# Kernel optimization log

Measured on AMD Instinct MI355X. Metric: run time of the kernel, lower is better.

Reference implementation:

```python
import jax, jax.numpy as jnp
import numpy as np
from jax import lax

B = 32768
N_INP = 256
N_HIDDEN = 1024
N_F = 256
N_ITERS = 100  # fixed-point solver iteration count in Convex


def _make_operators(n_f):
    # D = tridiag(-1, 2, -1) with first/last rows zeroed; mid = 0.5 * (sub+super diag ones)
    D = (-np.diag(np.ones(n_f - 1), -1) + 2 * np.diag(np.ones(n_f))
         - np.diag(np.ones(n_f - 1), 1)).astype(np.float32)
    D[0, :] = 0.0
    D[n_f - 1, :] = 0.0
    mid = 0.5 * (np.diag(np.ones(n_f - 1), -1) + np.diag(np.ones(n_f - 1), 1)).astype(np.float32)
    return jnp.asarray(D), jnp.asarray(mid)


def _convex(param):
    # param: [B, n_f]  (the torch code carries [B, n_f, 1]; column vec is equivalent)
    D, mid = _make_operators(param.shape[-1])

    def body(z, _):
        zx = z + param                       # [B, n_f]
        Dz = jnp.einsum('ij,bj->bi', D, zx)  # D @ zx
        mz = jnp.einsum('ij,bj->bi', mid, zx)
        dx = jnp.where(Dz > 0, zx - mz, 0.0)
        return zx - dx - param, None

    z0 = jnp.zeros_like(param)
    z_star, _ = lax.scan(body, z0, None, length=N_ITERS)
    return param + z_star  # Convex.forward: x + model(x)


def setup_inputs() -> dict:
    key = jax.random.key(0)
    k = jax.random.split(key, 5)
    x = jax.random.uniform(k[0], (B, N_INP + 1), dtype=jnp.float32)
    W1 = jax.random.normal(k[1], (N_HIDDEN, N_INP), dtype=jnp.float32) * 0.02
    b1 = jax.random.normal(k[2], (N_HIDDEN,), dtype=jnp.float32) * 0.02
    W2 = jax.random.normal(k[3], (N_F, N_HIDDEN), dtype=jnp.float32) * 0.02
    b2 = jax.random.normal(k[4], (N_F,), dtype=jnp.float32) * 0.02
    return {"x": x, "W1": W1, "b1": b1, "W2": W2, "b2": b2}


def reference(x, W1, b1, W2, b2):
    h = jax.nn.relu(x[..., :N_INP] @ W1.T + b1)     # [B, n_hidden]
    x_ = h @ W2.T + b2                              # [B, n_f]
    param = _convex(x_)                             # [B, n_f]
    # EvalConvex: round(query * (n_f - 1)) -> gather along feature dim
    idx = jnp.round(x[..., N_INP] * (N_F - 1)).astype(jnp.int32)  # [B]
    out = jnp.take_along_axis(param, idx[:, None], axis=1)        # [B, 1]
    return out.reshape(-1, 1, 1)                                  # [B, 1, 1]
```

## Files before the change

kernel.cpp:

```cpp
#include <hip/hip_runtime.h>
#include <stdint.h>

#define B_ROWS 32768
#define N_INP 256
#define N_HID 1024
#define NF 256
#define N_IT 100

typedef __attribute__((ext_vector_type(8))) _Float16 f16x8;
typedef __attribute__((ext_vector_type(4))) float f32x4;
typedef __attribute__((ext_vector_type(2))) _Float16 f16x2;
typedef float f32x4a __attribute__((ext_vector_type(4), aligned(4)));
typedef uint32_t u32;

__device__ __forceinline__ ushort f2h(float f) {
  _Float16 h = (_Float16)f;
  return *reinterpret_cast<ushort*>(&h);
}

__device__ __forceinline__ u32 pkh(float a, float b) {
  _Float16 ha = (_Float16)a, hb = (_Float16)b;
  return (u32)*reinterpret_cast<ushort*>(&ha) |
         ((u32)*reinterpret_cast<ushort*>(&hb) << 16);
}

__device__ __forceinline__ void async_copy16(const void* g, void* l) {
  __builtin_amdgcn_global_load_lds(
      (const __attribute__((address_space(1))) void*)g,
      (__attribute__((address_space(3))) void*)l, 16, 0, 0);
}

__device__ __forceinline__ f16x2 as_h2(u32 x) { return __builtin_bit_cast(f16x2, x); }
__device__ __forceinline__ u32 as_u32(f16x2 x) { return __builtin_bit_cast(u32, x); }
__device__ __forceinline__ f16x2 min2(f16x2 a, f16x2 b) {
  f16x2 r;
  asm("v_pk_min_f16 %0, %1, %2" : "=v"(r) : "v"(a), "v"(b));
  return r;
}

__global__ void prep_kernel(const float* __restrict__ x,
                            const float* __restrict__ W1,
                            const float* __restrict__ W2,
                            ushort* __restrict__ w1h,
                            ushort* __restrict__ w2h,
                            int* __restrict__ idx) {
  if (blockIdx.x < 256) {
    int t = blockIdx.x * 256 + threadIdx.x;
    float4 a = reinterpret_cast<const float4*>(W1)[t];
    float4 b = reinterpret_cast<const float4*>(W2)[t];
    reinterpret_cast<ushort4*>(w1h)[t] = make_ushort4(f2h(a.x), f2h(a.y), f2h(a.z), f2h(a.w));
    reinterpret_cast<ushort4*>(w2h)[t] = make_ushort4(f2h(b.x), f2h(b.y), f2h(b.z), f2h(b.w));
  } else {
    int r = (blockIdx.x - 256) * 256 + threadIdx.x;
    idx[r] = (int)rintf(x[(size_t)r * 257 + 256] * 255.0f);
  }
}

__global__ __launch_bounds__(256) void gemm1_x(
    const float* __restrict__ X,
    const ushort* __restrict__ Bw,
    const float* __restrict__ bias,
    ushort* __restrict__ C,
    int ntN) {
  __shared__ ushort As[2][128 * 64];
  __shared__ ushort Bs[2][128 * 64];
  const int t = threadIdx.x;
  const int w = t >> 6, l = t & 63;
  int bid = blockIdx.x;
  if (((int)gridDim.x & 7) == 0) {
    int cpx = (int)gridDim.x >> 3;
    bid = (bid & 7) * cpx + (bid >> 3);
  }
  const int tm = bid / ntN, tn = bid % ntN;
  const int wm = w >> 1, wn = w & 1;

  const float* Xb = X + (size_t)(tm * 128) * 257;
  const char* Bb = (const char*)(Bw + (size_t)tn * 128 * 256);
  const int sB = 512;
  const int lrow = l >> 3;
  const int lcol = (l & 7) * 16;

  const int ar0 = t >> 3;
  const int ak0 = (t & 7) * 8;

  f32x4a a0, a1, a2, a3, a4, a5, a6, a7;
#define LOADA(kt)                                                        \
  {                                                                      \
    const float* p0 = Xb + (size_t)ar0 * 257 + (kt) * 64 + ak0;          \
    const float* p1 = p0 + (size_t)32 * 257;                             \
    const float* p2 = p0 + (size_t)64 * 257;                             \
    const float* p3 = p0 + (size_t)96 * 257;                             \
    a0 = *(const f32x4a*)p0; a1 = *(const f32x4a*)(p0 + 4);              \
    a2 = *(const f32x4a*)p1; a3 = *(const f32x4a*)(p1 + 4);              \
    a4 = *(const f32x4a*)p2; a5 = *(const f32x4a*)(p2 + 4);              \
    a6 = *(const f32x4a*)p3; a7 = *(const f32x4a*)(p3 + 4);              \
  }
#define WRITEA(buf)                                                      \
  {                                                                      \
    uint4* d = (uint4*)((char*)&As[buf][0] + t * 16);                    \
    d[0]   = make_uint4(pkh(a0.x, a0.y), pkh(a0.z, a0.w),                \
                        pkh(a1.x, a1.y), pkh(a1.z, a1.w));               \
    d[256] = make_uint4(pkh(a2.x, a2.y), pkh(a2.z, a2.w),                \
                        pkh(a3.x, a3.y), pkh(a3.z, a3.w));               \
    d[512] = make_uint4(pkh(a4.x, a4.y), pkh(a4.z, a4.w),                \
                        pkh(a5.x, a5.y), pkh(a5.z, a5.w));               \
    d[768] = make_uint4(pkh(a6.x, a6.y), pkh(a6.z, a6.w),                \
                        pkh(a7.x, a7.y), pkh(a7.z, a7.w));               \
  }
#define STAGEB(kt, buf)                                                  \
  {                                                                      \
    const char* gb = Bb + lrow * sB + (kt) * 128 + lcol;                 \
    _Pragma("unroll") for (int i = 0; i < 4; ++i) {                      \
      int c = w * 4 + i;                                                 \
      async_copy16(gb + c * 8 * sB, (char*)&Bs[buf][0] + c * 1024);      \
    }                                                                    \
  }

  f32x4 acc[4][4];
#pragma unroll
  for (int i = 0; i < 4; ++i)
#pragma unroll
    for (int j = 0; j < 4; ++j) acc[i][j] = {0.f, 0.f, 0.f, 0.f};

  LOADA(0);
  STAGEB(0, 0);
  WRITEA(0);
  __syncthreads();

  const int arow = wm * 64 + (l & 15);
  const int brow = wn * 64 + (l & 15);
  const int koff = (l >> 4) * 8;

  for (int kt = 0; kt < 4; ++kt) {
    const int buf = kt & 1;
    if (kt < 3) {
      LOADA(kt + 1);
      STAGEB(kt + 1, buf ^ 1);
    }
#pragma unroll
    for (int ks = 0; ks < 2; ++ks) {
      f16x8 af[4], bfr[4];
#pragma unroll
      for (int mi = 0; mi < 4; ++mi)
        af[mi] = *(const f16x8*)&As[buf][(arow + mi * 16) * 64 + ks * 32 + koff];
#pragma unroll
      for (int ni = 0; ni < 4; ++ni)
        bfr[ni] = *(const f16x8*)&Bs[buf][(brow + ni * 16) * 64 + ks * 32 + koff];
#pragma unroll
      for (int mi = 0; mi < 4; ++mi)
#pragma unroll
        for (int ni = 0; ni < 4; ++ni)
          acc[mi][ni] = __builtin_amdgcn_mfma_f32_16x16x32_f16(
              af[mi], bfr[ni], acc[mi][ni], 0, 0, 0);
    }
    if (kt < 3) WRITEA(buf ^ 1);
    __syncthreads();
  }
#undef LOADA
#undef WRITEA
#undef STAGEB

  const int grow0 = tm * 128 + wm * 64 + (l >> 4) * 4;
  const int gcol0 = tn * 128 + wn * 64 + (l & 15);
#pragma unroll
  for (int ni = 0; ni < 4; ++ni) {
    const int col = gcol0 + ni * 16;
    const float bv = bias[col];
#pragma unroll
    for (int mi = 0; mi < 4; ++mi) {
      const int row = grow0 + mi * 16;
#pragma unroll
      for (int r = 0; r < 4; ++r) {
        float v = fmaxf(acc[mi][ni][r] + bv, 0.f);
        C[(size_t)(row + r) * N_HID + col] = f2h(v);
      }
    }
  }
}

__global__ __launch_bounds__(1024, 8) void gemm2_convex(
    const ushort* __restrict__ A,
    const ushort* __restrict__ Bw,
    const float* __restrict__ bias,
    const int* __restrict__ idxp,
    float* __restrict__ out) {
  __shared__ ushort smem[20480];
  const int tid = threadIdx.x;
  const int w = tid >> 6, l = tid & 63;
  const int wm = w >> 2, wn = w & 3;
  const int m0r = blockIdx.x * 64;

  f32x4 acc[4];
#pragma unroll
  for (int i = 0; i < 4; ++i) acc[i] = {0.f, 0.f, 0.f, 0.f};

  const int srow = tid >> 2;
  const int scs = (tid & 3) ^ ((srow >> 1) & 3);
  const ushort* gA = A + (size_t)(m0r + srow) * N_HID + scs * 8;
  const ushort* gB = Bw + (size_t)srow * N_HID + scs * 8;

#define STAGE(kt, buf)                                                  \
  {                                                                     \
    if (tid < 256) async_copy16(gA + (kt) * 32, smem + (buf) * 2048 + tid * 8); \
    async_copy16(gB + (kt) * 32, smem + 4096 + (buf) * 8192 + tid * 8); \
  }

  STAGE(0, 0);
  __syncthreads();

  const int arow = wm * 16 + (l & 15);
  const int brow0 = wn * 64 + (l & 15);
  const int kx = (((l >> 4) ^ ((l >> 1) & 3)) * 8);

  for (int kt = 0; kt < 32; ++kt) {
    const int buf = kt & 1;
    if (kt < 31) STAGE(kt + 1, buf ^ 1);
    f16x8 af = *(const f16x8*)(smem + buf * 2048 + arow * 32 + kx);
#pragma unroll
    for (int ni = 0; ni < 4; ++ni) {
      f16x8 bf = *(const f16x8*)(smem + 4096 + buf * 8192 + (brow0 + ni * 16) * 32 + kx);
      acc[ni] = __builtin_amdgcn_mfma_f32_16x16x32_f16(af, bf, acc[ni], 0, 0, 0);
    }
    __syncthreads();
  }
#undef STAGE

  {
    const int r0 = wm * 16 + (l >> 4) * 4;
    const int c0 = wn * 64 + (l & 15);
#pragma unroll
    for (int ni = 0; ni < 4; ++ni) {
      const int col = c0 + ni * 16;
      const float bv = bias[col];
#pragma unroll
      for (int r = 0; r < 4; ++r)
        smem[(r0 + r) * 256 + col] = f2h(acc[ni][r] + bv);
    }
  }
  __syncthreads();

  const int q = l & 15;
  const int row = w * 4 + (l >> 4);
  u32 w0, w1, w2, w3, w4, w5, w6, w7;
  {
    const uint4* src = reinterpret_cast<const uint4*>(smem + row * 256 + q * 16);
    uint4 v0 = src[0], v1 = src[1];
    w0 = v0.x; w1 = v0.y; w2 = v0.z; w3 = v0.w;
    w4 = v1.x; w5 = v1.y; w6 = v1.z; w7 = v1.w;
  }
  const int ii = idxp[m0r + row];
  const int upIdx = ((l - 1) & 63) * 4;
  const int dnIdx = ((l + 1) & 63) * 4;
  const bool fixP = (q == 0);
  const bool fixN = (q == 15);
  const f16x2 halfc = {(_Float16)0.5f, (_Float16)0.5f};

  u32 P = __builtin_amdgcn_ds_bpermute(upIdx, w7);
  u32 N = __builtin_amdgcn_ds_bpermute(dnIdx, w0);

#define AB(hi, lo) as_h2(__builtin_amdgcn_alignbit((hi), (lo), 16))
#define UPD(wj, sa, sb) wj = as_u32(min2(as_h2(wj), ((sa) + (sb)) * halfc))
#pragma unroll 2
  for (int it = 0; it < N_IT; ++it) {
    const u32 Pf = fixP ? 0x7C000000u : P;
    const u32 Nf = fixN ? 0x00007C00u : N;
    f16x2 s0 = AB(w0, Pf), s1 = AB(w1, w0), s2 = AB(w2, w1), s3 = AB(w3, w2);
    f16x2 s4 = AB(w4, w3), s5 = AB(w5, w4), s6 = AB(w6, w5), s7 = AB(w7, w6);
    f16x2 s8 = AB(Nf, w7);
    UPD(w7, s7, s8);
    UPD(w0, s0, s1);
    P = __builtin_amdgcn_ds_bpermute(upIdx, w7);
    N = __builtin_amdgcn_ds_bpermute(dnIdx, w0);
    UPD(w1, s1, s2); UPD(w2, s2, s3); UPD(w3, s3, s4);
    UPD(w4, s4, s5); UPD(w5, s5, s6); UPD(w6, s6, s7);
  }
#undef AB
#undef UPD

  const int sel = (ii >> 1) & 7;
  u32 a0 = (sel & 4) ? w4 : w0, a1 = (sel & 4) ? w5 : w1;
  u32 a2 = (sel & 4) ? w6 : w2, a3 = (sel & 4) ? w7 : w3;
  u32 b0 = (sel & 2) ? a2 : a0, b1 = (sel & 2) ? a3 : a1;
  u32 c0 = (sel & 1) ? b1 : b0;
  ushort hv = (ii & 1) ? (ushort)(c0 >> 16) : (ushort)(c0 & 0xffffu);
  float v = (float)__builtin_bit_cast(_Float16, hv);
  v = __shfl(v, (l & ~15) | (ii >> 4));
  if (q == 0) out[m0r + row] = v;
}

extern "C" void kernel_launch(void* const* d_in, const int* in_sizes, int n_in,
                              void* d_out, int out_size, void* d_ws, size_t ws_size,
                              hipStream_t stream) {
  const float* x = (const float*)d_in[0];
  const float* W1 = (const float*)d_in[1];
  const float* b1 = (const float*)d_in[2];
  const float* W2 = (const float*)d_in[3];
  const float* b2 = (const float*)d_in[4];
  float* out = (float*)d_out;

  char* ws = (char*)d_ws;
  ushort* w1h = (ushort*)ws;
  ushort* w2h = (ushort*)(ws + 524288);
  int*    idx = (int*)  (ws + 1048576);
  ushort* h   = (ushort*)(ws + 1179648);

  const size_t fixed = 1179648;
  int chunk = 2048;
  if (ws_size >= fixed + (size_t)32768 * 2048) chunk = 32768;
  else if (ws_size >= fixed + (size_t)16384 * 2048) chunk = 16384;
  else if (ws_size >= fixed + (size_t)8192 * 2048) chunk = 8192;
  else if (ws_size >= fixed + (size_t)4096 * 2048) chunk = 4096;

  prep_kernel<<<384, 256, 0, stream>>>(x, W1, W2, w1h, w2h, idx);

  for (int m0 = 0; m0 < B_ROWS; m0 += chunk) {
    int curM = (B_ROWS - m0 < chunk) ? (B_ROWS - m0) : chunk;
    dim3 g1((curM / 128) * (N_HID / 128));
    gemm1_x<<<g1, 256, 0, stream>>>(x + (size_t)m0 * 257, w1h, b1, h,
                                    N_HID / 128);
    gemm2_convex<<<curM / 64, 1024, 0, stream>>>(h, w2h, b2, idx + m0, out + m0);
  }
}
```

Before: 122.5 us.

## Merge GEMM1 and GEMM2+convex into one software-pipelined kernel over chunks

Replaces the separate gemm1 and gemm2_convex launches with a single kernel. Each launch runs gemm1 for chunk k and gemm2+convex for chunk k-1 at the same time, using a double-buffered hidden workspace. The goal is to overlap the ALU-heavy convex iteration with the MFMA/memory-bound first GEMM and to shrink chunk sizes for better L2 locality. Gemm1 is rewritten for 1024-thread blocks with smaller per-wave tiles (32x32) and swizzled LDS. The cost is extra launches (nch+1) and less register reuse per wave in gemm1.

After: 219.1 us. +78.8%, slower.

```diff
diff --git a/kernel.cpp b/kernel.cpp
--- a/kernel.cpp
+++ b/kernel.cpp
@@ -56,148 +56,34 @@
   }
 }
 
-__global__ __launch_bounds__(256) void gemm1_x(
-    const float* __restrict__ X,
-    const ushort* __restrict__ Bw,
-    const float* __restrict__ bias,
-    ushort* __restrict__ C,
-    int ntN) {
-  __shared__ ushort As[2][128 * 64];
-  __shared__ ushort Bs[2][128 * 64];
-  const int t = threadIdx.x;
-  const int w = t >> 6, l = t & 63;
-  int bid = blockIdx.x;
-  if (((int)gridDim.x & 7) == 0) {
-    int cpx = (int)gridDim.x >> 3;
-    bid = (bid & 7) * cpx + (bid >> 3);
-  }
-  const int tm = bid / ntN, tn = bid % ntN;
-  const int wm = w >> 1, wn = w & 1;
-
-  const float* Xb = X + (size_t)(tm * 128) * 257;
-  const char* Bb = (const char*)(Bw + (size_t)tn * 128 * 256);
-  const int sB = 512;
-  const int lrow = l >> 3;
-  const int lcol = (l & 7) * 16;
-
-  const int ar0 = t >> 3;
-  const int ak0 = (t & 7) * 8;
-
-  f32x4a a0, a1, a2, a3, a4, a5, a6, a7;
-#define LOADA(kt)                                                        \
-  {                                                                      \
-    const float* p0 = Xb + (size_t)ar0 * 257 + (kt) * 64 + ak0;          \
-    const float* p1 = p0 + (size_t)32 * 257;                             \
-    const float* p2 = p0 + (size_t)64 * 257;                             \
-    const float* p3 = p0 + (size_t)96 * 257;                             \
-    a0 = *(const f32x4a*)p0; a1 = *(const f32x4a*)(p0 + 4);              \
-    a2 = *(const f32x4a*)p1; a3 = *(const f32x4a*)(p1 + 4);              \
-    a4 = *(const f32x4a*)p2; a5 = *(const f32x4a*)(p2 + 4);              \
-    a6 = *(const f32x4a*)p3; a7 = *(const f32x4a*)(p3 + 4);              \
-  }
-#define WRITEA(buf)                                                      \
-  {                                                                      \
-    uint4* d = (uint4*)((char*)&As[buf][0] + t * 16);                    \
-    d[0]   = make_uint4(pkh(a0.x, a0.y), pkh(a0.z, a0.w),                \
-                        pkh(a1.x, a1.y), pkh(a1.z, a1.w));               \
-    d[256] = make_uint4(pkh(a2.x, a2.y), pkh(a2.z, a2.w),                \
-                        pkh(a3.x, a3.y), pkh(a3.z, a3.w));               \
-    d[512] = make_uint4(pkh(a4.x, a4.y), pkh(a4.z, a4.w),                \
-                        pkh(a5.x, a5.y), pkh(a5.z, a5.w));               \
-    d[768] = make_uint4(pkh(a6.x, a6.y), pkh(a6.z, a6.w),                \
-                        pkh(a7.x, a7.y), pkh(a7.z, a7.w));               \
-  }
-#define STAGEB(kt, buf)                                                  \
-  {                                                                      \
-    const char* gb = Bb + lrow * sB + (kt) * 128 + lcol;                 \
-    _Pragma("unroll") for (int i = 0; i < 4; ++i) {                      \
-      int c = w * 4 + i;                                                 \
-      async_copy16(gb + c * 8 * sB, (char*)&Bs[buf][0] + c * 1024);      \
-    }                                                                    \
-  }
-
-  f32x4 acc[4][4];
-#pragma unroll
-  for (int i = 0; i < 4; ++i)
-#pragma unroll
-    for (int j = 0; j < 4; ++j) acc[i][j] = {0.f, 0.f, 0.f, 0.f};
-
-  LOADA(0);
-  STAGEB(0, 0);
-  WRITEA(0);
-  __syncthreads();
-
-  const int arow = wm * 64 + (l & 15);
-  const int brow = wn * 64 + (l & 15);
-  const int koff = (l >> 4) * 8;
-
-  for (int kt = 0; kt < 4; ++kt) {
-    const int buf = kt & 1;
-    if (kt < 3) {
-      LOADA(kt + 1);
-      STAGEB(kt + 1, buf ^ 1);
-    }
-#pragma unroll
-    for (int ks = 0; ks < 2; ++ks) {
-      f16x8 af[4], bfr[4];
-#pragma unroll
-      for (int mi = 0; mi < 4; ++mi)
-        af[mi] = *(const f16x8*)&As[buf][(arow + mi * 16) * 64 + ks * 32 + koff];
-#pragma unroll
-      for (int ni = 0; ni < 4; ++ni)
-        bfr[ni] = *(const f16x8*)&Bs[buf][(brow + ni * 16) * 64 + ks * 32 + koff];
-#pragma unroll
-      for (int mi = 0; mi < 4; ++mi)
-#pragma unroll
-        for (int ni = 0; ni < 4; ++ni)
-          acc[mi][ni] = __builtin_amdgcn_mfma_f32_16x16x32_f16(
-              af[mi], bfr[ni], acc[mi][ni], 0, 0, 0);
-    }
-    if (kt < 3) WRITEA(buf ^ 1);
-    __syncthreads();
-  }
-#undef LOADA
-#undef WRITEA
-#undef STAGEB
-
-  const int grow0 = tm * 128 + wm * 64 + (l >> 4) * 4;
-  const int gcol0 = tn * 128 + wn * 64 + (l & 15);
-#pragma unroll
-  for (int ni = 0; ni < 4; ++ni) {
-    const int col = gcol0 + ni * 16;
-    const float bv = bias[col];
-#pragma unroll
-    for (int mi = 0; mi < 4; ++mi) {
-      const int row = grow0 + mi * 16;
-#pragma unroll
-      for (int r = 0; r < 4; ++r) {
-        float v = fmaxf(acc[mi][ni][r] + bv, 0.f);
-        C[(size_t)(row + r) * N_HID + col] = f2h(v);
-      }
-    }
-  }
-}
-
-__global__ __launch_bounds__(1024, 8) void gemm2_convex(
-    const ushort* __restrict__ A,
-    const ushort* __restrict__ Bw,
-    const float* __restrict__ bias,
+__global__ __launch_bounds__(1024, 8) void mega(
+    const float* __restrict__ Xg1,
+    const ushort* __restrict__ w1h,
+    const float* __restrict__ b1,
+    ushort* __restrict__ Hw,
+    const ushort* __restrict__ Hr,
+    const ushort* __restrict__ w2h,
+    const float* __restrict__ b2,
     const int* __restrict__ idxp,
-    float* __restrict__ out) {
-  __shared__ ushort smem[20480];
+    float* __restrict__ outp,
+    int nG2) {
+  __shared__ char smraw[40960];
   const int tid = threadIdx.x;
   const int w = tid >> 6, l = tid & 63;
-  const int wm = w >> 2, wn = w & 3;
-  const int m0r = blockIdx.x * 64;
-
-  f32x4 acc[4];
-#pragma unroll
-  for (int i = 0; i < 4; ++i) acc[i] = {0.f, 0.f, 0.f, 0.f};
-
-  const int srow = tid >> 2;
-  const int scs = (tid & 3) ^ ((srow >> 1) & 3);
-  const ushort* gA = A + (size_t)(m0r + srow) * N_HID + scs * 8;
-  const ushort* gB = Bw + (size_t)srow * N_HID + scs * 8;
+
+  if ((int)blockIdx.x < nG2) {
+    ushort* smem = (ushort*)smraw;
+    const int wm = w >> 2, wn = w & 3;
+    const int m0r = blockIdx.x * 64;
+
+    f32x4 acc[4];
+#pragma unroll
+    for (int i = 0; i < 4; ++i) acc[i] = {0.f, 0.f, 0.f, 0.f};
+
+    const int srow = tid >> 2;
+    const int scs = (tid & 3) ^ ((srow >> 1) & 3);
+    const ushort* gA = Hr + (size_t)(m0r + srow) * N_HID + scs * 8;
+    const ushort* gB = w2h + (size_t)srow * N_HID + scs * 8;
 
 #define STAGE(kt, buf)                                                  \
   {                                                                     \
@@ -205,87 +91,155 @@
     async_copy16(gB + (kt) * 32, smem + 4096 + (buf) * 8192 + tid * 8); \
   }
 
-  STAGE(0, 0);
-  __syncthreads();
-
-  const int arow = wm * 16 + (l & 15);
-  const int brow0 = wn * 64 + (l & 15);
-  const int kx = (((l >> 4) ^ ((l >> 1) & 3)) * 8);
-
-  for (int kt = 0; kt < 32; ++kt) {
-    const int buf = kt & 1;
-    if (kt < 31) STAGE(kt + 1, buf ^ 1);
-    f16x8 af = *(const f16x8*)(smem + buf * 2048 + arow * 32 + kx);
-#pragma unroll
-    for (int ni = 0; ni < 4; ++ni) {
-      f16x8 bf = *(const f16x8*)(smem + 4096 + buf * 8192 + (brow0 + ni * 16) * 32 + kx);
-      acc[ni] = __builtin_amdgcn_mfma_f32_16x16x32_f16(af, bf, acc[ni], 0, 0, 0);
-    }
+    STAGE(0, 0);
     __syncthreads();
-  }
+
+    const int arow = wm * 16 + (l & 15);
+    const int brow0 = wn * 64 + (l & 15);
+    const int kx = (((l >> 4) ^ ((l >> 1) & 3)) * 8);
+
+    for (int kt = 0; kt < 32; ++kt) {
+      const int buf = kt & 1;
+      if (kt < 31) STAGE(kt + 1, buf ^ 1);
+      f16x8 af = *(const f16x8*)(smem + buf * 2048 + arow * 32 + kx);
+#pragma unroll
+      for (int ni = 0; ni < 4; ++ni) {
+        f16x8 bf = *(const f16x8*)(smem + 4096 + buf * 8192 + (brow0 + ni * 16) * 32 + kx);
+        acc[ni] = __builtin_amdgcn_mfma_f32_16x16x32_f16(af, bf, acc[ni], 0, 0, 0);
+      }
+      __syncthreads();
+    }
 #undef STAGE
 
-  {
-    const int r0 = wm * 16 + (l >> 4) * 4;
-    const int c0 = wn * 64 + (l & 15);
-#pragma unroll
-    for (int ni = 0; ni < 4; ++ni) {
-      const int col = c0 + ni * 16;
-      const float bv = bias[col];
-#pragma unroll
-      for (int r = 0; r < 4; ++r)
-        smem[(r0 + r) * 256 + col] = f2h(acc[ni][r] + bv);
-    }
-  }
-  __syncthreads();
-
-  const int q = l & 15;
-  const int row = w * 4 + (l >> 4);
-  u32 w0, w1, w2, w3, w4, w5, w6, w7;
-  {
-    const uint4* src = reinterpret_cast<const uint4*>(smem + row * 256 + q * 16);
-    uint4 v0 = src[0], v1 = src[1];
-    w0 = v0.x; w1 = v0.y; w2 = v0.z; w3 = v0.w;
-    w4 = v1.x; w5 = v1.y; w6 = v1.z; w7 = v1.w;
-  }
-  const int ii = idxp[m0r + row];
-  const int upIdx = ((l - 1) & 63) * 4;
-  const int dnIdx = ((l + 1) & 63) * 4;
-  const bool fixP = (q == 0);
-  const bool fixN = (q == 15);
-  const f16x2 halfc = {(_Float16)0.5f, (_Float16)0.5f};
-
-  u32 P = __builtin_amdgcn_ds_bpermute(upIdx, w7);
-  u32 N = __builtin_amdgcn_ds_bpermute(dnIdx, w0);
+    {
+      const int r0 = wm * 16 + (l >> 4) * 4;
+      const int c0 = wn * 64 + (l & 15);
+#pragma unroll
+      for (int ni = 0; ni < 4; ++ni) {
+        const int col = c0 + ni * 16;
+        const float bv = b2[col];
+#pragma unroll
+        for (int r = 0; r < 4; ++r)
+          smem[(r0 + r) * 256 + col] = f2h(acc[ni][r] + bv);
+      }
+    }
+    __syncthreads();
+
+    const int q = l & 15;
+    const int row = w * 4 + (l >> 4);
+    u32 w0, w1, w2, w3, w4, w5, w6, w7;
+    {
+      const uint4* src = reinterpret_cast<const uint4*>(smem + row * 256 + q * 16);
+      uint4 v0 = src[0], v1 = src[1];
+      w0 = v0.x; w1 = v0.y; w2 = v0.z; w3 = v0.w;
+      w4 = v1.x; w5 = v1.y; w6 = v1.z; w7 = v1.w;
+    }
+    const int ii = idxp[m0r + row];
+    const int upIdx = ((l - 1) & 63) * 4;
+    const int dnIdx = ((l + 1) & 63) * 4;
+    const bool fixP = (q == 0);
+    const bool fixN = (q == 15);
+    const f16x2 halfc = {(_Float16)0.5f, (_Float16)0.5f};
+
+    u32 P = __builtin_amdgcn_ds_bpermute(upIdx, w7);
+    u32 N = __builtin_amdgcn_ds_bpermute(dnIdx, w0);
 
 #define AB(hi, lo) as_h2(__builtin_amdgcn_alignbit((hi), (lo), 16))
 #define UPD(wj, sa, sb) wj = as_u32(min2(as_h2(wj), ((sa) + (sb)) * halfc))
 #pragma unroll 2
-  for (int it = 0; it < N_IT; ++it) {
-    const u32 Pf = fixP ? 0x7C000000u : P;
-    const u32 Nf = fixN ? 0x00007C00u : N;
-    f16x2 s0 = AB(w0, Pf), s1 = AB(w1, w0), s2 = AB(w2, w1), s3 = AB(w3, w2);
-    f16x2 s4 = AB(w4, w3), s5 = AB(w5, w4), s6 = AB(w6, w5), s7 = AB(w7, w6);
-    f16x2 s8 = AB(Nf, w7);
-    UPD(w7, s7, s8);
-    UPD(w0, s0, s1);
-    P = __builtin_amdgcn_ds_bpermute(upIdx, w7);
-    N = __builtin_amdgcn_ds_bpermute(dnIdx, w0);
-    UPD(w1, s1, s2); UPD(w2, s2, s3); UPD(w3, s3, s4);
-    UPD(w4, s4, s5); UPD(w5, s5, s6); UPD(w6, s6, s7);
-  }
+    for (int it = 0; it < N_IT; ++it) {
+      const u32 Pf = fixP ? 0x7C000000u : P;
+      const u32 Nf = fixN ? 0x00007C00u : N;
+      f16x2 s0 = AB(w0, Pf), s1 = AB(w1, w0), s2 = AB(w2, w1), s3 = AB(w3, w2);
+      f16x2 s4 = AB(w4, w3), s5 = AB(w5, w4), s6 = AB(w6, w5), s7 = AB(w7, w6);
+      f16x2 s8 = AB(Nf, w7);
+      UPD(w7, s7, s8);
+      UPD(w0, s0, s1);
+      P = __builtin_amdgcn_ds_bpermute(upIdx, w7);
+      N = __builtin_amdgcn_ds_bpermute(dnIdx, w0);
+      UPD(w1, s1, s2); UPD(w2, s2, s3); UPD(w3, s3, s4);
+      UPD(w4, s4, s5); UPD(w5, s5, s6); UPD(w6, s6, s7);
+    }
 #undef AB
 #undef UPD
 
-  const int sel = (ii >> 1) & 7;
-  u32 a0 = (sel & 4) ? w4 : w0, a1 = (sel & 4) ? w5 : w1;
-  u32 a2 = (sel & 4) ? w6 : w2, a3 = (sel & 4) ? w7 : w3;
-  u32 b0 = (sel & 2) ? a2 : a0, b1 = (sel & 2) ? a3 : a1;
-  u32 c0 = (sel & 1) ? b1 : b0;
-  ushort hv = (ii & 1) ? (ushort)(c0 >> 16) : (ushort)(c0 & 0xffffu);
-  float v = (float)__builtin_bit_cast(_Float16, hv);
-  v = __shfl(v, (l & ~15) | (ii >> 4));
-  if (q == 0) out[m0r + row] = v;
+    const int sel = (ii >> 1) & 7;
+    u32 a0 = (sel & 4) ? w4 : w0, a1 = (sel & 4) ? w5 : w1;
+    u32 a2 = (sel & 4) ? w6 : w2, a3 = (sel & 4) ? w7 : w3;
+    u32 b0 = (sel & 2) ? a2 : a0, b1s = (sel & 2) ? a3 : a1;
+    u32 c0 = (sel & 1) ? b1s : b0;
+    ushort hv = (ii & 1) ? (ushort)(c0 >> 16) : (ushort)(c0 & 0xffffu);
+    float v = (float)__builtin_bit_cast(_Float16, hv);
+    v = __shfl(v, (l & ~15) | (ii >> 4));
+    if (q == 0) outp[m0r + row] = v;
+
+  } else {
+    const int rb = (int)blockIdx.x - nG2;
+    const int tm = rb >> 3, tn = rb & 7;
+    const float* Xb = Xg1 + (size_t)(tm * 128) * 257;
+    const ushort* Bt = w1h + (size_t)(tn * 128) * 256;
+    char* As = smraw;
+    char* Bs = smraw + 16384;
+
+    const int sra = tid >> 3;
+    const int ha = tid & 7;
+    const int gca = (((ha >> 1) ^ (sra & 3)) << 3) + ((ha & 1) << 2);
+    const int srb = tid >> 2;
+    const int cb = (((tid & 3) ^ (srb & 3)) << 3);
+
+    f32x4a av;
+    f32x4 acc00 = {0.f, 0.f, 0.f, 0.f}, acc01 = {0.f, 0.f, 0.f, 0.f};
+    f32x4 acc10 = {0.f, 0.f, 0.f, 0.f}, acc11 = {0.f, 0.f, 0.f, 0.f};
+
+#define LOADA1(kt) av = *(const f32x4a*)(Xb + (size_t)sra * 257 + (kt) * 32 + gca);
+#define WRITEA1(buf)                                                     \
+    *(uint2*)(As + (buf) * 8192 + tid * 8) =                             \
+        make_uint2(pkh(av.x, av.y), pkh(av.z, av.w));
+#define STAGEB1(kt, buf)                                                 \
+    if (tid < 512)                                                       \
+      async_copy16(Bt + (size_t)srb * 256 + (kt) * 32 + cb,              \
+                   Bs + (buf) * 8192 + tid * 16);
+
+    LOADA1(0);
+    STAGEB1(0, 0);
+    WRITEA1(0);
+    __syncthreads();
+
+    const int wmg = w >> 2, wng = w & 3;
+    const int lr = l & 15;
+    const int kxb = (((l >> 4) ^ (l & 3)) << 4);
+    const int ra0 = (wmg * 32 + lr) * 64 + kxb;
+    const int rbo = (wng * 32 + lr) * 64 + kxb;
+
+    for (int kt = 0; kt < 8; ++kt) {
+      const int buf = kt & 1;
+      if (kt < 7) { LOADA1(kt + 1); STAGEB1(kt + 1, buf ^ 1); }
+      f16x8 a0 = *(const f16x8*)(As + buf * 8192 + ra0);
+      f16x8 a1 = *(const f16x8*)(As + buf * 8192 + ra0 + 16 * 64);
+      f16x8 bf0 = *(const f16x8*)(Bs + buf * 8192 + rbo);
+      f16x8 bf1 = *(const f16x8*)(Bs + buf * 8192 + rbo + 16 * 64);
+      acc00 = __builtin_amdgcn_mfma_f32_16x16x32_f16(a0, bf0, acc00, 0, 0, 0);
+      acc01 = __builtin_amdgcn_mfma_f32_16x16x32_f16(a0, bf1, acc01, 0, 0, 0);
+      acc10 = __builtin_amdgcn_mfma_f32_16x16x32_f16(a1, bf0, acc10, 0, 0, 0);
+      acc11 = __builtin_amdgcn_mfma_f32_16x16x32_f16(a1, bf1, acc11, 0, 0, 0);
+      if (kt < 7) WRITEA1(buf ^ 1);
+      __syncthreads();
+    }
+#undef LOADA1
+#undef WRITEA1
+#undef STAGEB1
+
+    const int grow0 = tm * 128 + wmg * 32 + (l >> 4) * 4;
+    const int gcol0 = tn * 128 + wng * 32 + lr;
+    const float bv0 = b1[gcol0], bv1 = b1[gcol0 + 16];
+#pragma unroll
+    for (int r = 0; r < 4; ++r) {
+      Hw[(size_t)(grow0 + r) * N_HID + gcol0] = f2h(fmaxf(acc00[r] + bv0, 0.f));
+      Hw[(size_t)(grow0 + r) * N_HID + gcol0 + 16] = f2h(fmaxf(acc01[r] + bv1, 0.f));
+      Hw[(size_t)(grow0 + 16 + r) * N_HID + gcol0] = f2h(fmaxf(acc10[r] + bv0, 0.f));
+      Hw[(size_t)(grow0 + 16 + r) * N_HID + gcol0 + 16] = f2h(fmaxf(acc11[r] + bv1, 0.f));
+    }
+  }
 }
 
 extern "C" void kernel_launch(void* const* d_in, const int* in_sizes, int n_in,
@@ -302,22 +256,25 @@
   ushort* w1h = (ushort*)ws;
   ushort* w2h = (ushort*)(ws + 524288);
   int*    idx = (int*)  (ws + 1048576);
-  ushort* h   = (ushort*)(ws + 1179648);
+  ushort* hbuf = (ushort*)(ws + 1179648);
 
   const size_t fixed = 1179648;
   int chunk = 2048;
-  if (ws_size >= fixed + (size_t)32768 * 2048) chunk = 32768;
-  else if (ws_size >= fixed + (size_t)16384 * 2048) chunk = 16384;
-  else if (ws_size >= fixed + (size_t)8192 * 2048) chunk = 8192;
-  else if (ws_size >= fixed + (size_t)4096 * 2048) chunk = 4096;
+  if (ws_size >= fixed + 2 * (size_t)8192 * 2048) chunk = 8192;
+  else if (ws_size >= fixed + 2 * (size_t)4096 * 2048) chunk = 4096;
 
   prep_kernel<<<384, 256, 0, stream>>>(x, W1, W2, w1h, w2h, idx);
 
-  for (int m0 = 0; m0 < B_ROWS; m0 += chunk) {
-    int curM = (B_ROWS - m0 < chunk) ? (B_ROWS - m0) : chunk;
-    dim3 g1((curM / 128) * (N_HID / 128));
-    gemm1_x<<<g1, 256, 0, stream>>>(x + (size_t)m0 * 257, w1h, b1, h,
-                                    N_HID / 128);
-    gemm2_convex<<<curM / 64, 1024, 0, stream>>>(h, w2h, b2, idx + m0, out + m0);
-  }
-}
+  const int nch = B_ROWS / chunk;
+  for (int k = 0; k <= nch; ++k) {
+    const int nG1 = (k < nch) ? (chunk / 128) * (N_HID / 128) : 0;
+    const int nG2 = (k > 0) ? chunk / 64 : 0;
+    const int kw = (k < nch) ? k : 0;
+    const int kr = (k > 0) ? (k - 1) : 0;
+    ushort* hw = hbuf + (size_t)(kw & 1) * chunk * 1024;
+    ushort* hr = hbuf + (size_t)(kr & 1) * chunk * 1024;
+    mega<<<nG1 + nG2, 1024, 0, stream>>>(
+        x + (size_t)kw * chunk * 257, w1h, b1, hw,
+        hr, w2h, b2, idx + (size_t)kr * chunk, out + (size_t)kr * chunk, nG2);
+  }
+}
```
